# Kernel optimization log

Hardware: AMD Instinct MI355X
Metric: run time of the kernel (lower is better)

## Reference

```python
import jax, jax.numpy as jnp
import numpy as np

N_QUBITS = 8
DIM = 1 << N_QUBITS  # 256 basis states


def _cnot_chain_perm(n):
    # Compose CNOT(0,1)..CNOT(n-2,n-1), CNOT(n-1,0) as a single basis permutation.
    # Convention: wire 0 is the most-significant bit of the basis index.
    idx = np.arange(1 << n)
    f = idx.copy()
    pairs = [(w, w + 1) for w in range(n - 1)] + [(n - 1, 0)]
    for c, t in pairs:
        ctrl = (f >> (n - 1 - c)) & 1
        f = np.where(ctrl == 1, f ^ (1 << (n - 1 - t)), f)
    finv = np.empty_like(f)
    finv[f] = idx  # new_state = old_state[finv]
    return finv

_PERM = jnp.asarray(_cnot_chain_perm(N_QUBITS))
# sign[s, i] = +1 if bit i of basis state s is 0 else -1 (PauliZ eigenvalue)
_SIGN = jnp.asarray(
    1.0 - 2.0 * (((np.arange(DIM)[:, None] >> (N_QUBITS - 1 - np.arange(N_QUBITS))[None, :]) & 1)),
    dtype=np.float32,
)


def _qgate(x, theta):
    """Simulated circuit: RX(x_i) encoder + trainable RX(theta_i) + CNOT ring + <Z_i>.
    RX(x)RX(theta) = RX(x+theta); each qubit amplitude is cos or -i*sin, so basis
    probabilities are real products of cos^2/sin^2, permuted by the CNOT chain.
    x: (B, n) angles, theta: (n,). Returns (B, n) Pauli-Z expectations."""
    alpha = 0.5 * (x + theta)
    p = jnp.stack([jnp.cos(alpha) ** 2, jnp.sin(alpha) ** 2], axis=-1)  # (B, n, 2)
    probs = p[:, 0]  # (B, 2)
    for i in range(1, N_QUBITS):  # outer product over wires -> (B, 2^n)
        probs = (probs[:, :, None] * p[:, i][:, None, :]).reshape(probs.shape[0], -1)
    probs = probs[:, _PERM]  # apply CNOT ring (pure basis permutation)
    return probs @ _SIGN


def setup_inputs() -> dict:
    key = jax.random.key(0)
    ks = jax.random.split(key, 8)
    T, B, D, H, Q = 256, 512, 256, 256, N_QUBITS
    s = lambda k, shape, scale: jax.random.normal(k, shape, jnp.float32) * scale
    return {
        "inputs": jax.random.normal(ks[0], (T, B, D), jnp.float32),
        "W_proj": s(ks[1], (D + H, 4 * Q), 0.05),
        "b_proj": jnp.zeros((4 * Q,), jnp.float32),
        "theta_gate": s(ks[2], (Q,), 1.0),
        "W_qproj": s(ks[3], (Q, H), 0.3),
        "b_qproj": jnp.zeros((H,), jnp.float32),
        "theta_attn": s(ks[4], (Q,), 1.0),
        "W_attn_proj": s(ks[5], (H, Q), 0.05),
        "b_attn_proj": jnp.zeros((Q,), jnp.float32),
        "W_attn_back": s(ks[6], (Q, H), 0.3),
        "b_attn_back": jnp.zeros((H,), jnp.float32),
    }


def reference(inputs, W_proj, b_proj, theta_gate, W_qproj, b_qproj,
              theta_attn, W_attn_proj, b_attn_proj, W_attn_back, b_attn_back):
    T, B, _ = inputs.shape
    H = W_qproj.shape[1]
    hx0 = jnp.zeros((B, H), inputs.dtype)
    cx0 = jnp.zeros((B, H), inputs.dtype)

    def step(carry, x):
        hx, cx = carry
        gates = jnp.concatenate([x, hx], axis=1) @ W_proj + b_proj  # (B, 4*Q)
        f_in, i_in, g_in, o_in = jnp.split(gates, 4, axis=1)
        qp = lambda z: _qgate(z, theta_gate) @ W_qproj + b_qproj
        f = jax.nn.sigmoid(qp(f_in))
        i = jax.nn.sigmoid(qp(i_in))
        g = jnp.tanh(qp(g_in))
        o = jax.nn.sigmoid(qp(o_in))
        cx = f * cx + i * g
        hx = o * jnp.tanh(cx)
        hq = _qgate(hx @ W_attn_proj + b_attn_proj, theta_attn)  # quantum attention
        hx = hq @ W_attn_back + b_attn_back
        return (hx, cx), hx

    (hx, cx), outs = jax.lax.scan(step, (hx0, cx0), inputs)
    return outs, (hx, cx)
```

## Files before the change

### kernel.cpp

```cpp
#include <hip/hip_runtime.h>

#define T_STEPS 256
#define BATCH   512
#define DIN     256
#define HDIM    256

typedef unsigned int u32;
typedef _Float16 h2 __attribute__((ext_vector_type(2)));

__device__ __forceinline__ u32 pack2(float a, float b) {
    return __builtin_bit_cast(u32, __builtin_amdgcn_cvt_pkrtz(a, b));
}
__device__ __forceinline__ float dot2(u32 a, u32 b, float acc) {
    return __builtin_amdgcn_fdot2(__builtin_bit_cast(h2, a),
                                  __builtin_bit_cast(h2, b), acc, false);
}
__device__ __forceinline__ float rcpf(float x) { return __builtin_amdgcn_rcpf(x); }
__device__ __forceinline__ float fast_sigmoid(float x) {
    return rcpf(1.0f + __expf(-x));
}
__device__ __forceinline__ float fast_tanh(float x) {
    return 1.0f - 2.0f * rcpf(__expf(2.0f * x) + 1.0f);
}

template<int CTRL>
__device__ __forceinline__ float dppf(float x) {
    int xi = __builtin_bit_cast(int, x);
    return __builtin_bit_cast(float,
        __builtin_amdgcn_update_dpp(xi, xi, CTRL, 0xF, 0xF, false));
}
#define DPP_XOR1  0xB1
#define DPP_XOR2  0x4E
#define DPP_HMIR  0x141
#define DPP_SHR1  0x111
#define DPP_SHR2  0x112
#define DPP_SHR4  0x114
#define DPP_SHL1  0x101

__device__ __forceinline__ void lds_barrier() {
    asm volatile("s_waitcnt lgkmcnt(0)\n\ts_barrier" ::: "memory");
}

__launch_bounds__(256, 2)
__global__ void qlstm_fused(const float* __restrict__ inputs,
                            const float* __restrict__ W_proj,
                            const float* __restrict__ b_proj,
                            const float* __restrict__ theta_gate,
                            const float* __restrict__ W_qproj,
                            const float* __restrict__ b_qproj,
                            const float* __restrict__ theta_attn,
                            const float* __restrict__ W_attn_proj,
                            const float* __restrict__ b_attn_proj,
                            const float* __restrict__ W_attn_back,
                            const float* __restrict__ b_attn_back,
                            float* __restrict__ out) {
    const int tid  = threadIdx.x;
    const int b    = blockIdx.x;
    const int w    = tid >> 6;
    const int lw   = tid & 63;
    const int g    = lw & 31;
    const int q    = lw & 7;
    const int o    = lw >> 3;

    __shared__ __align__(16) u32 hS[128];
    __shared__ __align__(16) u32 xS[256];
    __shared__ __align__(16) u32 hmS[160];
    __shared__ __align__(16) u32 ogS[64];
    __shared__ __align__(16) float caS[32];
    __shared__ __align__(16) float preS[256];

    u32 WxP[16], WhP[16];
    {
        const int dbase = 64 * w + (lw >> 5) * 32;
        #pragma unroll
        for (int i = 0; i < 16; ++i) {
            WxP[i] = pack2(W_proj[(dbase + 2 * i) * 32 + g],
                           W_proj[(dbase + 2 * i + 1) * 32 + g]);
            WhP[i] = pack2(W_proj[(DIN + dbase + 2 * i) * 32 + g],
                           W_proj[(DIN + dbase + 2 * i + 1) * 32 + g]);
        }
    }
    u32 WqpP[4];
    #pragma unroll
    for (int p = 0; p < 4; ++p)
        WqpP[p] = pack2(W_qproj[(2 * p) * HDIM + tid],
                        W_qproj[(2 * p + 1) * HDIM + tid]);
    u32 WapP[16];
    #pragma unroll
    for (int i = 0; i < 16; ++i)
        WapP[i] = pack2(W_attn_proj[(32 * q + 2 * i) * 8 + o],
                        W_attn_proj[(32 * q + 2 * i + 1) * 8 + o]);
    u32 WabP[4];
    #pragma unroll
    for (int p = 0; p < 4; ++p)
        WabP[p] = pack2(W_attn_back[(2 * p) * HDIM + tid],
                        W_attn_back[(2 * p + 1) * HDIM + tid]);
    const float bqp  = b_qproj[tid];
    const float bap  = b_attn_proj[o] + theta_attn[o];
    const float bab  = b_attn_back[tid];
    const float bias = b_proj[g] + theta_gate[g & 7];

    if (tid < 128) hS[tid] = 0u;
    {
        float x0  = inputs[(size_t)b * DIN + tid];
        float x0n = dppf<DPP_SHL1>(x0);
        if (!(tid & 1)) xS[tid >> 1] = pack2(x0, x0n);
    }
    float cx = 0.f, hx = 0.f;
    __syncthreads();

    for (int t = 0; t < T_STEPS; ++t) {
        const int xb = (t & 1) << 7;
        float xn = 0.f;
        if (t + 1 < T_STEPS)
            xn = inputs[((size_t)(t + 1) * BATCH + b) * DIN + tid];

        const int sbase = 32 * w + (lw >> 5) * 16;
        const uint4* xp = (const uint4*)&xS[xb + sbase];
        const uint4* hp = (const uint4*)&hS[sbase];
        uint4 x0 = xp[0], x1 = xp[1], x2 = xp[2], x3 = xp[3];
        uint4 v0 = hp[0], v1 = hp[1], v2 = hp[2], v3 = hp[3];
        float a0 = dot2(x0.x, WxP[ 0], 0.f);
        a0 = dot2(x0.y, WxP[ 1], a0);
        a0 = dot2(x0.z, WxP[ 2], a0);
        a0 = dot2(x0.w, WxP[ 3], a0);
        float a1 = dot2(x1.x, WxP[ 4], 0.f);
        a1 = dot2(x1.y, WxP[ 5], a1);
        a1 = dot2(x1.z, WxP[ 6], a1);
        a1 = dot2(x1.w, WxP[ 7], a1);
        float a2 = dot2(x2.x, WxP[ 8], 0.f);
        a2 = dot2(x2.y, WxP[ 9], a2);
        a2 = dot2(x2.z, WxP[10], a2);
        a2 = dot2(x2.w, WxP[11], a2);
        float a3 = dot2(x3.x, WxP[12], 0.f);
        a3 = dot2(x3.y, WxP[13], a3);
        a3 = dot2(x3.z, WxP[14], a3);
        a3 = dot2(x3.w, WxP[15], a3);
        float a4 = dot2(v0.x, WhP[ 0], 0.f);
        a4 = dot2(v0.y, WhP[ 1], a4);
        a4 = dot2(v0.z, WhP[ 2], a4);
        a4 = dot2(v0.w, WhP[ 3], a4);
        float a5 = dot2(v1.x, WhP[ 4], 0.f);
        a5 = dot2(v1.y, WhP[ 5], a5);
        a5 = dot2(v1.z, WhP[ 6], a5);
        a5 = dot2(v1.w, WhP[ 7], a5);
        float a6 = dot2(v2.x, WhP[ 8], 0.f);
        a6 = dot2(v2.y, WhP[ 9], a6);
        a6 = dot2(v2.z, WhP[10], a6);
        a6 = dot2(v2.w, WhP[11], a6);
        float a7 = dot2(v3.x, WhP[12], 0.f);
        a7 = dot2(v3.y, WhP[13], a7);
        a7 = dot2(v3.z, WhP[14], a7);
        a7 = dot2(v3.w, WhP[15], a7);
        float part = ((a0 + a1) + (a2 + a3)) + ((a4 + a5) + (a6 + a7));
        preS[w * 64 + lw] = part;
        lds_barrier();
        float pre = (((preS[g      ] + preS[ 32 + g]) +
                      (preS[64 + g ] + preS[ 96 + g])) +
                     ((preS[128 + g] + preS[160 + g]) +
                      (preS[192 + g] + preS[224 + g]))) + bias;
        float cq = __cosf(pre);

        float s = cq;
        { float u1 = dppf<DPP_SHR1>(s); if (q >= 1) s *= u1; }
        { float u2 = dppf<DPP_SHR2>(s); if (q >= 2) s *= u2; }
        { float u4 = dppf<DPP_SHR4>(s); if (q >= 4) s *= u4; }
        float v = (q == 0) ? 1.0f : cq;
        v *= dppf<DPP_XOR1>(v);
        v *= dppf<DPP_XOR2>(v);
        v *= dppf<DPP_HMIR>(v);
        float outv = (q == 0) ? v : s;
        float onx  = dppf<DPP_SHL1>(outv);
        if (lw < 32 && !(lw & 1))
            ogS[w * 16 + (lw >> 1)] = pack2(outv, onx);

        const uint4* ogp = (const uint4*)&ogS[w * 16];
        uint4 og0 = ogp[0], og1 = ogp[1], og2 = ogp[2], og3 = ogp[3];
        float d0 = dot2(og0.x, WqpP[0], bqp);
        d0 = dot2(og0.y, WqpP[1], d0);
        d0 = dot2(og0.z, WqpP[2], d0);
        d0 = dot2(og0.w, WqpP[3], d0);
        float d1 = dot2(og1.x, WqpP[0], bqp);
        d1 = dot2(og1.y, WqpP[1], d1);
        d1 = dot2(og1.z, WqpP[2], d1);
        d1 = dot2(og1.w, WqpP[3], d1);
        float d2 = dot2(og2.x, WqpP[0], bqp);
        d2 = dot2(og2.y, WqpP[1], d2);
        d2 = dot2(og2.z, WqpP[2], d2);
        d2 = dot2(og2.w, WqpP[3], d2);
        float d3 = dot2(og3.x, WqpP[0], bqp);
        d3 = dot2(og3.y, WqpP[1], d3);
        d3 = dot2(og3.z, WqpP[2], d3);
        d3 = dot2(og3.w, WqpP[3], d3);
        float fv = fast_sigmoid(d0);
        float iv = fast_sigmoid(d1);
        float gv = fast_tanh(d2);
        float ov = fast_sigmoid(d3);
        cx = fmaf(fv, cx, iv * gv);
        float hm = ov * fast_tanh(cx);
        float hmn = dppf<DPP_SHL1>(hm);
        if (!(tid & 1))
            hmS[(tid >> 5) * 20 + ((tid >> 1) & 15)] = pack2(hm, hmn);
        lds_barrier();

        const uint4* mp = (const uint4*)&hmS[q * 20];
        uint4 m0 = mp[0], m1 = mp[1], m2 = mp[2], m3 = mp[3];
        float s0 = dot2(m0.x, WapP[ 0], 0.f);
        s0 = dot2(m0.y, WapP[ 1], s0);
        s0 = dot2(m0.z, WapP[ 2], s0);
        s0 = dot2(m0.w, WapP[ 3], s0);
        float s1 = dot2(m1.x, WapP[ 4], 0.f);
        s1 = dot2(m1.y, WapP[ 5], s1);
        s1 = dot2(m1.z, WapP[ 6], s1);
        s1 = dot2(m1.w, WapP[ 7], s1);
        float s2 = dot2(m2.x, WapP[ 8], 0.f);
        s2 = dot2(m2.y, WapP[ 9], s2);
        s2 = dot2(m2.z, WapP[10], s2);
        s2 = dot2(m2.w, WapP[11], s2);
        float s3 = dot2(m3.x, WapP[12], 0.f);
        s3 = dot2(m3.y, WapP[13], s3);
        s3 = dot2(m3.z, WapP[14], s3);
        s3 = dot2(m3.w, WapP[15], s3);
        float sd = (s0 + s1) + (s2 + s3);
        sd += dppf<DPP_XOR1>(sd);
        sd += dppf<DPP_XOR2>(sd);
        sd += dppf<DPP_HMIR>(sd);
        float co = __cosf(sd + bap);
        if (!(lw & 7)) caS[w * 8 + o] = co;

        float4 cA = *(const float4*)&caS[w * 8];
        float4 cB = *(const float4*)&caS[w * 8 + 4];
        float p1 = cA.x * cA.y;
        float p2 = p1 * cA.z;
        float p3 = p2 * cA.w;
        float p4 = p3 * cB.x;
        float p5 = p4 * cB.y;
        float p6 = p5 * cB.z;
        float p7 = p6 * cB.w;
        float q12 = cA.y * cA.z, q34 = cA.w * cB.x, q56 = cB.y * cB.z;
        float p0 = (q12 * q34) * (q56 * cB.w);
        u32 oq0 = pack2(p0, p1);
        u32 oq1 = pack2(p2, p3);
        u32 oq2 = pack2(p4, p5);
        u32 oq3 = pack2(p6, p7);
        float hv = dot2(oq0, WabP[0], bab);
        hv = dot2(oq1, WabP[1], hv);
        hv = dot2(oq2, WabP[2], hv);
        hv = dot2(oq3, WabP[3], hv);
        hx = hv;
        out[((size_t)t * BATCH + b) * HDIM + tid] = hx;
        float hxn = dppf<DPP_SHL1>(hx);
        if (!(tid & 1))
            hS[tid >> 1] = pack2(hx, hxn);
        {
            float xnx = dppf<DPP_SHL1>(xn);
            if (!(tid & 1)) xS[(xb ^ 128) + (tid >> 1)] = pack2(xn, xnx);
        }
    }

    const size_t base = (size_t)T_STEPS * BATCH * HDIM;
    out[base + (size_t)b * HDIM + tid] = hx;
    out[base + (size_t)BATCH * HDIM + (size_t)b * HDIM + tid] = cx;
}

extern "C" void kernel_launch(void* const* d_in, const int* in_sizes, int n_in,
                              void* d_out, int out_size, void* d_ws, size_t ws_size,
                              hipStream_t stream) {
    const float* inputs      = (const float*)d_in[0];
    const float* W_proj      = (const float*)d_in[1];
    const float* b_proj      = (const float*)d_in[2];
    const float* theta_gate  = (const float*)d_in[3];
    const float* W_qproj     = (const float*)d_in[4];
    const float* b_qproj     = (const float*)d_in[5];
    const float* theta_attn  = (const float*)d_in[6];
    const float* W_attn_proj = (const float*)d_in[7];
    const float* b_attn_proj = (const float*)d_in[8];
    const float* W_attn_back = (const float*)d_in[9];
    const float* b_attn_back = (const float*)d_in[10];
    float* outp = (float*)d_out;

    qlstm_fused<<<BATCH, 256, 0, stream>>>(
        inputs, W_proj, b_proj, theta_gate, W_qproj, b_qproj, theta_attn,
        W_attn_proj, b_attn_proj, W_attn_back, b_attn_back, outp);
}
```

Measured before the change: 286.9 us.

## Precompute next step's input projection off the recurrent critical path

Moves the x-dependent half of the gate projection out of the head of each timestep and computes it for step t+1 in the middle of step t, after the attention cosine. Only the h-dependent dot products then remain on the serial dependency chain. The double-buffered xS array becomes a single buffer. The write and reread of xS rely on the existing barrier placement, which risks a race between the write and the reads by other threads.

```diff
diff --git a/kernel.cpp b/kernel.cpp
--- a/kernel.cpp
+++ b/kernel.cpp
@@ -63,7 +63,7 @@
     const int o    = lw >> 3;
 
     __shared__ __align__(16) u32 hS[128];
-    __shared__ __align__(16) u32 xS[256];
+    __shared__ __align__(16) u32 xS[128];
     __shared__ __align__(16) u32 hmS[160];
     __shared__ __align__(16) u32 ogS[64];
     __shared__ __align__(16) float caS[32];
@@ -109,17 +109,11 @@
     float cx = 0.f, hx = 0.f;
     __syncthreads();
 
-    for (int t = 0; t < T_STEPS; ++t) {
-        const int xb = (t & 1) << 7;
-        float xn = 0.f;
-        if (t + 1 < T_STEPS)
-            xn = inputs[((size_t)(t + 1) * BATCH + b) * DIN + tid];
-
-        const int sbase = 32 * w + (lw >> 5) * 16;
-        const uint4* xp = (const uint4*)&xS[xb + sbase];
-        const uint4* hp = (const uint4*)&hS[sbase];
+    const int sbase = 32 * w + (lw >> 5) * 16;
+    float partX;
+    {
+        const uint4* xp = (const uint4*)&xS[sbase];
         uint4 x0 = xp[0], x1 = xp[1], x2 = xp[2], x3 = xp[3];
-        uint4 v0 = hp[0], v1 = hp[1], v2 = hp[2], v3 = hp[3];
         float a0 = dot2(x0.x, WxP[ 0], 0.f);
         a0 = dot2(x0.y, WxP[ 1], a0);
         a0 = dot2(x0.z, WxP[ 2], a0);
@@ -136,6 +130,16 @@
         a3 = dot2(x3.y, WxP[13], a3);
         a3 = dot2(x3.z, WxP[14], a3);
         a3 = dot2(x3.w, WxP[15], a3);
+        partX = (a0 + a1) + (a2 + a3);
+    }
+
+    for (int t = 0; t < T_STEPS; ++t) {
+        float xn = 0.f;
+        if (t + 1 < T_STEPS)
+            xn = inputs[((size_t)(t + 1) * BATCH + b) * DIN + tid];
+
+        const uint4* hp = (const uint4*)&hS[sbase];
+        uint4 v0 = hp[0], v1 = hp[1], v2 = hp[2], v3 = hp[3];
         float a4 = dot2(v0.x, WhP[ 0], 0.f);
         a4 = dot2(v0.y, WhP[ 1], a4);
         a4 = dot2(v0.z, WhP[ 2], a4);
@@ -152,11 +156,11 @@
         a7 = dot2(v3.y, WhP[13], a7);
         a7 = dot2(v3.z, WhP[14], a7);
         a7 = dot2(v3.w, WhP[15], a7);
-        float part = ((a0 + a1) + (a2 + a3)) + ((a4 + a5) + (a6 + a7));
+        float part = ((a4 + a5) + (a6 + a7)) + partX;
         preS[w * 64 + lw] = part;
         lds_barrier();
         float pre = (((preS[g      ] + preS[ 32 + g]) +
-                      (preS[64 + g ] + preS[ 96 + g])) +
+                      (preS[ 64 + g] + preS[ 96 + g])) +
                      ((preS[128 + g] + preS[160 + g]) +
                       (preS[192 + g] + preS[224 + g]))) + bias;
         float cq = __cosf(pre);
@@ -228,6 +232,30 @@
         float co = __cosf(sd + bap);
         if (!(lw & 7)) caS[w * 8 + o] = co;
 
+        {
+            float xnx = dppf<DPP_SHL1>(xn);
+            if (!(tid & 1)) xS[tid >> 1] = pack2(xn, xnx);
+            const uint4* xp2 = (const uint4*)&xS[sbase];
+            uint4 y0 = xp2[0], y1 = xp2[1], y2 = xp2[2], y3 = xp2[3];
+            float b0 = dot2(y0.x, WxP[ 0], 0.f);
+            b0 = dot2(y0.y, WxP[ 1], b0);
+            b0 = dot2(y0.z, WxP[ 2], b0);
+            b0 = dot2(y0.w, WxP[ 3], b0);
+            float b1 = dot2(y1.x, WxP[ 4], 0.f);
+            b1 = dot2(y1.y, WxP[ 5], b1);
+            b1 = dot2(y1.z, WxP[ 6], b1);
+            b1 = dot2(y1.w, WxP[ 7], b1);
+            float b2 = dot2(y2.x, WxP[ 8], 0.f);
+            b2 = dot2(y2.y, WxP[ 9], b2);
+            b2 = dot2(y2.z, WxP[10], b2);
+            b2 = dot2(y2.w, WxP[11], b2);
+            float b3 = dot2(y3.x, WxP[12], 0.f);
+            b3 = dot2(y3.y, WxP[13], b3);
+            b3 = dot2(y3.z, WxP[14], b3);
+            b3 = dot2(y3.w, WxP[15], b3);
+            partX = (b0 + b1) + (b2 + b3);
+        }
+
         float4 cA = *(const float4*)&caS[w * 8];
         float4 cB = *(const float4*)&caS[w * 8 + 4];
         float p1 = cA.x * cA.y;
@@ -252,10 +280,6 @@
         float hxn = dppf<DPP_SHL1>(hx);
         if (!(tid & 1))
             hS[tid >> 1] = pack2(hx, hxn);
-        {
-            float xnx = dppf<DPP_SHL1>(xn);
-            if (!(tid & 1)) xS[(xb ^ 128) + (tid >> 1)] = pack2(xn, xnx);
-        }
     }
 
     const size_t base = (size_t)T_STEPS * BATCH * HDIM;
```

Measured after the change: 279.9 us. 2.4% less time.
